# Kernel tuning notes

Measured on AMD Instinct MI355X. Metric: run time of the kernel, lower is better.

Reference implementation:

```python
import jax, jax.numpy as jnp
import numpy as np


def _rbf_forward(batches, centers, beta, W, b):
    # Pairwise Euclidean distances via GEMM expansion instead of materializing
    # the O(n*K*dim) difference tensor the torch code builds.
    x2 = jnp.sum(batches * batches, axis=1, keepdims=True)          # [n, 1]
    c2 = jnp.sum(centers * centers, axis=1)                          # [K]
    xc = jnp.einsum('nd,kd->nk', batches, centers)                   # [n, K]
    d2 = jnp.maximum(x2 + c2[None, :] - 2.0 * xc, 0.0)               # [n, K]
    dist = jnp.sqrt(d2)
    radial = jnp.exp(-beta * dist)                                   # beta: [1, K]
    return radial @ W.T + b                                          # [n, num_class]


def setup_inputs() -> dict:
    key = jax.random.key(0)
    k1, k2, k3, k4, k5 = jax.random.split(key, 5)
    n, K, dim, num_class = 16384, 2048, 512, 10
    batches = jax.random.normal(k1, (n, dim), dtype=jnp.float32)
    centers = jax.random.normal(k2, (K, dim), dtype=jnp.float32)
    beta = jnp.full((1, K), 0.1, dtype=jnp.float32)  # torch init: ones/10
    W = jax.random.normal(k4, (num_class, K), dtype=jnp.float32) / np.sqrt(K)
    b = jax.random.normal(k5, (num_class,), dtype=jnp.float32) * 0.01
    return {"batches": batches, "centers": centers, "beta": beta, "W": W, "b": b}


def reference(batches, centers, beta, W, b):
    return _rbf_forward(batches, centers, beta, W, b)
```

## Files before the change

kernel.cpp:

```cpp
#include <hip/hip_runtime.h>
#include <hip/hip_bf16.h>
#include <stdint.h>

#define M_N  16384
#define K_C  2048
#define DIM  512
#define NCLS 10
#define NBN  16
#define NBM  (M_N / 128)

typedef unsigned short u16;
typedef float  f32x4  __attribute__((ext_vector_type(4)));
typedef __bf16 bf16x8 __attribute__((ext_vector_type(8)));


__device__ __forceinline__ void async_ld16(const void* g, void* l) {
  __builtin_amdgcn_global_load_lds(
      (const __attribute__((address_space(1))) void*)g,
      (__attribute__((address_space(3))) void*)l,
      16, 0, 0);
}

__device__ __forceinline__ u16 f2bf_rne(float f) {
  uint32_t u = __float_as_uint(f);
  u += 0x7FFFu + ((u >> 16) & 1u);
  return (u16)(u >> 16);
}


#define NPREP ((M_N + K_C) / 2)

__global__ __launch_bounds__(256) void prep(
    const float4* __restrict__ batches, const float4* __restrict__ centers,
    const float* __restrict__ W,
    ushort4* __restrict__ Abf, ushort4* __restrict__ Bbf,
    float* __restrict__ x2, float* __restrict__ c2, u16* __restrict__ Wbf) {
  int b = blockIdx.x, t = threadIdx.x;
  if (b < NPREP) {
    int rp = b * 2 + (t >> 7);
    int col = t & 127;
    const float4* src; ushort4* dst; float* sq; int row;
    if (rp < M_N) { src = batches; dst = Abf; sq = x2; row = rp; }
    else          { src = centers; dst = Bbf; sq = c2; row = rp - M_N; }
    float4 v = src[(size_t)row * 128 + col];
    float ss = v.x * v.x + v.y * v.y + v.z * v.z + v.w * v.w;
    ushort4 o;
    o.x = f2bf_rne(v.x); o.y = f2bf_rne(v.y);
    o.z = f2bf_rne(v.z); o.w = f2bf_rne(v.w);
    dst[(size_t)row * 128 + col] = o;
    ss += __shfl_down(ss, 32);
    ss += __shfl_down(ss, 16);
    ss += __shfl_down(ss, 8);
    ss += __shfl_down(ss, 4);
    ss += __shfl_down(ss, 2);
    ss += __shfl_down(ss, 1);
    __shared__ float part[4];
    if ((t & 63) == 0) part[t >> 6] = ss;
    __syncthreads();
    if (t == 0) sq[row] = part[0] + part[1];
    if (t == 128) sq[row] = part[2] + part[3];
  } else {
    int wb = b - NPREP;
#pragma unroll
    for (int i = 0; i < 4; ++i) {
      int idx = wb * 1024 + i * 256 + t;
      int n = idx >> 11, k = idx & 2047;
      Wbf[idx] = (n < NCLS) ? f2bf_rne(W[n * K_C + k]) : (u16)0;
    }
  }
}


__global__ __launch_bounds__(256, 4) void rbf_main(
    const u16* __restrict__ A,
    const u16* __restrict__ B,
    const float* __restrict__ x2,
    const float* __restrict__ c2,
    const float* __restrict__ beta,
    const u16* __restrict__ Wbf,
    float* __restrict__ partial) {
  constexpr int BK = 64;
  __shared__ alignas(16) unsigned char smem[32768];
  u16* As = (u16*)smem;
  u16* Bs = (u16*)(smem + 16384);
  u16* Rt = (u16*)smem;

  const int tid  = threadIdx.x;
  const int lane = tid & 63;
  const int wid  = tid >> 6;
  const int bid = blockIdx.x;
  const int g = bid >> 3, r8 = bid & 7;
  const int bm = r8 * 16 + (g & 15);
  const int bn = g >> 4;
  const int row0 = bm * 128, col0 = bn * 128;
  const int wrC = (wid >> 1) * 64;
  const int wcB = (wid & 1) * 64;

  f32x4 acc[4][4] = {};

  const int srow = tid >> 3;
  const int scol = ((tid & 7) ^ (srow & 7)) * 8;
  const u16* aG = A + (size_t)(row0 + srow) * DIM + scol;
  const u16* bG = B + (size_t)(col0 + srow) * DIM + scol;
  u16* aL = As + tid * 8;
  u16* bL = Bs + tid * 8;

  const int frow = lane & 15;
  const int fq   = lane >> 4;
  const int fsw  = frow & 7;

  for (int k0 = 0; k0 < DIM; k0 += BK) {
    __syncthreads();
#pragma unroll
    for (int i = 0; i < 4; ++i) {
      async_ld16(aG + k0 + i * 32 * DIM, aL + i * 2048);
      async_ld16(bG + k0 + i * 32 * DIM, bL + i * 2048);
    }
    __syncthreads();

#pragma unroll
    for (int kh = 0; kh < 2; ++kh) {
      const int slot = ((kh << 2) | fq) ^ fsw;
      bf16x8 cf[4], bfr[4];
#pragma unroll
      for (int mi = 0; mi < 4; ++mi)
        cf[mi] = *(const bf16x8*)(Bs + (wrC + mi * 16 + frow) * BK + slot * 8);
#pragma unroll
      for (int ni = 0; ni < 4; ++ni)
        bfr[ni] = *(const bf16x8*)(As + (wcB + ni * 16 + frow) * BK + slot * 8);
#pragma unroll
      for (int mi = 0; mi < 4; ++mi)
#pragma unroll
        for (int ni = 0; ni < 4; ++ni)
          acc[mi][ni] = __builtin_amdgcn_mfma_f32_16x16x32_bf16(
              cf[mi], bfr[ni], acc[mi][ni], 0, 0, 0);
    }
  }

  const int cls = lane & 15, q = lane >> 4;
  float4 c2q[4], btq[4];
#pragma unroll
  for (int mi = 0; mi < 4; ++mi) {
    int base = col0 + wrC + mi * 16 + q * 4;
    c2q[mi] = *(const float4*)(c2 + base);
    btq[mi] = *(const float4*)(beta + base);
  }
  float x2v[4];
#pragma unroll
  for (int ni = 0; ni < 4; ++ni)
    x2v[ni] = x2[row0 + wcB + ni * 16 + cls];

  __syncthreads();

  union Pack { u16 h[4]; uint2 v; };
#pragma unroll
  for (int mi = 0; mi < 4; ++mi) {
#pragma unroll
    for (int ni = 0; ni < 4; ++ni) {
      Pack pk;
#pragma unroll
      for (int r = 0; r < 4; ++r) {
        float xc = acc[mi][ni][r];
        float d2 = fmaxf(x2v[ni] + c2q[mi][r] - 2.0f * xc, 0.0f);
        float radial = __expf(-btq[mi][r] * sqrtf(d2));
        pk.h[r] = f2bf_rne(radial);
      }
      int br  = wcB + ni * 16 + cls;
      int cc0 = wrC + mi * 16 + q * 4;
      *(uint2*)(Rt + br * 128 + (cc0 ^ ((br & 15) << 3))) = pk.v;
    }
  }
  __syncthreads();

  bf16x8 wfr[4];
#pragma unroll
  for (int t = 0; t < 4; ++t)
    wfr[t] = *(const bf16x8*)(Wbf + (size_t)cls * K_C + col0 + t * 32 + q * 8);

  f32x4 acc2[2] = {};
#pragma unroll
  for (int s2 = 0; s2 < 2; ++s2) {
    const int br = (wid * 2 + s2) * 16 + cls;
    const u16* rrow = Rt + br * 128;
    const int sw = cls << 3;
#pragma unroll
    for (int t = 0; t < 4; ++t) {
      bf16x8 ra = *(const bf16x8*)(rrow + ((t * 32 + q * 8) ^ sw));
      acc2[s2] = __builtin_amdgcn_mfma_f32_16x16x32_bf16(
          ra, wfr[t], acc2[s2], 0, 0, 0);
    }
  }

#pragma unroll
  for (int s2 = 0; s2 < 2; ++s2)
#pragma unroll
    for (int r = 0; r < 4; ++r) {
      int gr = row0 + (wid * 2 + s2) * 16 + q * 4 + r;
      partial[((size_t)bn * M_N + gr) * 16 + cls] = acc2[s2][r];
    }
}


__global__ __launch_bounds__(256) void reduce_out(
    const float* __restrict__ partial, const float* __restrict__ b,
    float* __restrict__ out) {
  int t = threadIdx.x;
  int row = blockIdx.x * 64 + (t >> 2);
  int quad = t & 3;
  float4 v = {0.f, 0.f, 0.f, 0.f};
#pragma unroll
  for (int bn = 0; bn < NBN; ++bn) {
    float4 p = *(const float4*)(partial + ((size_t)bn * M_N + row) * 16 + quad * 4);
    v.x += p.x; v.y += p.y; v.z += p.z; v.w += p.w;
  }
  if (quad == 0) {
    float4 bq = *(const float4*)b;
    float* o = out + (size_t)row * NCLS;
    *(float2*)o       = {v.x + bq.x, v.y + bq.y};
    *(float2*)(o + 2) = {v.z + bq.z, v.w + bq.w};
  } else if (quad == 1) {
    float4 bq = *(const float4*)(b + 4);
    float* o = out + (size_t)row * NCLS + 4;
    *(float2*)o       = {v.x + bq.x, v.y + bq.y};
    *(float2*)(o + 2) = {v.z + bq.z, v.w + bq.w};
  } else if (quad == 2) {
    *(float2*)(out + (size_t)row * NCLS + 8) = {v.x + b[8], v.y + b[9]};
  }
}


extern "C" void kernel_launch(void* const* d_in, const int* in_sizes, int n_in,
                              void* d_out, int out_size, void* d_ws, size_t ws_size,
                              hipStream_t stream) {
  const float* batches = (const float*)d_in[0];
  const float* centers = (const float*)d_in[1];
  const float* beta    = (const float*)d_in[2];
  const float* W       = (const float*)d_in[3];
  const float* bias    = (const float*)d_in[4];
  float* out = (float*)d_out;

  char* ws = (char*)d_ws;
  u16*  Abf = (u16*)ws;
  u16*  Bbf = (u16*)(ws + (size_t)M_N * DIM * 2);
  float* x2 = (float*)(ws + (size_t)(M_N + K_C) * DIM * 2);
  float* c2 = x2 + M_N;
  u16*  Wbf = (u16*)(c2 + K_C);
  float* partial = (float*)((char*)Wbf + 16 * K_C * 2);

  prep<<<dim3(NPREP + 32), dim3(256), 0, stream>>>(
      (const float4*)batches, (const float4*)centers, W,
      (ushort4*)Abf, (ushort4*)Bbf, x2, c2, Wbf);
  rbf_main<<<dim3(NBN * NBM), dim3(256), 0, stream>>>(
      Abf, Bbf, x2, c2, beta, Wbf, partial);
  reduce_out<<<dim3(M_N / 64), dim3(256), 0, stream>>>(partial, bias, out);
}
```

Baseline: 145.8 us.

## Feed radial values to second MFMA from registers via permuted W, skip LDS round-trip

```diff
diff --git a/kernel.cpp b/kernel.cpp
--- a/kernel.cpp
+++ b/kernel.cpp
@@ -34,7 +34,7 @@
     const float4* __restrict__ batches, const float4* __restrict__ centers,
     const float* __restrict__ W,
     ushort4* __restrict__ Abf, ushort4* __restrict__ Bbf,
-    float* __restrict__ x2, float* __restrict__ c2, u16* __restrict__ Wbf) {
+    float* __restrict__ x2, float* __restrict__ c2, u16* __restrict__ Wperm) {
   int b = blockIdx.x, t = threadIdx.x;
   if (b < NPREP) {
     int rp = b * 2 + (t >> 7);
@@ -63,9 +63,13 @@
     int wb = b - NPREP;
 #pragma unroll
     for (int i = 0; i < 4; ++i) {
-      int idx = wb * 1024 + i * 256 + t;
-      int n = idx >> 11, k = idx & 2047;
-      Wbf[idx] = (n < NCLS) ? f2bf_rne(W[n * K_C + k]) : (u16)0;
+      int p = wb * 1024 + i * 256 + t;
+      int cls = p >> 11, k = p & 2047;
+      int bn = k >> 7, rem = k & 127;
+      int hh = (rem >> 6) & 1, tt = (rem >> 5) & 1;
+      int qq = (rem >> 3) & 3, jj = rem & 7;
+      int c = bn * 128 + hh * 64 + (tt * 2 + (jj >> 2)) * 16 + qq * 4 + (jj & 3);
+      Wperm[p] = (cls < NCLS) ? f2bf_rne(W[cls * K_C + c]) : (u16)0;
     }
   }
 }
@@ -77,13 +81,13 @@
     const float* __restrict__ x2,
     const float* __restrict__ c2,
     const float* __restrict__ beta,
-    const u16* __restrict__ Wbf,
+    const u16* __restrict__ Wperm,
     float* __restrict__ partial) {
   constexpr int BK = 64;
   __shared__ alignas(16) unsigned char smem[32768];
   u16* As = (u16*)smem;
   u16* Bs = (u16*)(smem + 16384);
-  u16* Rt = (u16*)smem;
+  f32x4* sumbuf = (f32x4*)smem;
 
   const int tid  = threadIdx.x;
   const int lane = tid & 63;
@@ -150,54 +154,60 @@
   for (int ni = 0; ni < 4; ++ni)
     x2v[ni] = x2[row0 + wcB + ni * 16 + cls];
 
-  __syncthreads();
-
-  union Pack { u16 h[4]; uint2 v; };
-#pragma unroll
-  for (int mi = 0; mi < 4; ++mi) {
-#pragma unroll
-    for (int ni = 0; ni < 4; ++ni) {
-      Pack pk;
+#pragma unroll
+  for (int mi = 0; mi < 4; ++mi)
+#pragma unroll
+    for (int ni = 0; ni < 4; ++ni)
 #pragma unroll
       for (int r = 0; r < 4; ++r) {
         float xc = acc[mi][ni][r];
         float d2 = fmaxf(x2v[ni] + c2q[mi][r] - 2.0f * xc, 0.0f);
-        float radial = __expf(-btq[mi][r] * sqrtf(d2));
-        pk.h[r] = f2bf_rne(radial);
+        acc[mi][ni][r] = __expf(-btq[mi][r] * sqrtf(d2));
       }
-      int br  = wcB + ni * 16 + cls;
-      int cc0 = wrC + mi * 16 + q * 4;
-      *(uint2*)(Rt + br * 128 + (cc0 ^ ((br & 15) << 3))) = pk.v;
-    }
-  }
+
+  const int h = wid >> 1;
+  bf16x8 wfr[2];
+#pragma unroll
+  for (int t = 0; t < 2; ++t)
+    wfr[t] = *(const bf16x8*)(Wperm + (size_t)cls * K_C + col0 + h * 64 +
+                              t * 32 + q * 8);
+
+  f32x4 acc2[4] = {};
+#pragma unroll
+  for (int ni = 0; ni < 4; ++ni) {
+#pragma unroll
+    for (int t = 0; t < 2; ++t) {
+      union { u16 hh[8]; bf16x8 v; } pk;
+#pragma unroll
+      for (int r = 0; r < 4; ++r) {
+        pk.hh[r]     = f2bf_rne(acc[2 * t][ni][r]);
+        pk.hh[4 + r] = f2bf_rne(acc[2 * t + 1][ni][r]);
+      }
+      acc2[ni] = __builtin_amdgcn_mfma_f32_16x16x32_bf16(
+          pk.v, wfr[t], acc2[ni], 0, 0, 0);
+    }
+  }
+
   __syncthreads();
-
-  bf16x8 wfr[4];
-#pragma unroll
-  for (int t = 0; t < 4; ++t)
-    wfr[t] = *(const bf16x8*)(Wbf + (size_t)cls * K_C + col0 + t * 32 + q * 8);
-
-  f32x4 acc2[2] = {};
-#pragma unroll
-  for (int s2 = 0; s2 < 2; ++s2) {
-    const int br = (wid * 2 + s2) * 16 + cls;
-    const u16* rrow = Rt + br * 128;
-    const int sw = cls << 3;
-#pragma unroll
-    for (int t = 0; t < 4; ++t) {
-      bf16x8 ra = *(const bf16x8*)(rrow + ((t * 32 + q * 8) ^ sw));
-      acc2[s2] = __builtin_amdgcn_mfma_f32_16x16x32_bf16(
-          ra, wfr[t], acc2[s2], 0, 0, 0);
-    }
-  }
-
-#pragma unroll
-  for (int s2 = 0; s2 < 2; ++s2)
-#pragma unroll
-    for (int r = 0; r < 4; ++r) {
-      int gr = row0 + (wid * 2 + s2) * 16 + q * 4 + r;
-      partial[((size_t)bn * M_N + gr) * 16 + cls] = acc2[s2][r];
-    }
+  if (wid >= 2) {
+#pragma unroll
+    for (int ni = 0; ni < 4; ++ni)
+      sumbuf[((wid & 1) * 4 + ni) * 64 + lane] = acc2[ni];
+  }
+  __syncthreads();
+  if (wid < 2) {
+#pragma unroll
+    for (int ni = 0; ni < 4; ++ni) {
+      f32x4 o = sumbuf[(wid * 4 + ni) * 64 + lane];
+      acc2[ni] += o;
+#pragma unroll
+      for (int r = 0; r < 4; ++r) {
+        int gr = row0 + wid * 64 + ni * 16 + q * 4 + r;
+        __builtin_nontemporal_store(
+            acc2[ni][r], &partial[((size_t)bn * M_N + gr) * 16 + cls]);
+      }
+    }
+  }
 }
 
 
@@ -207,11 +217,12 @@
   int t = threadIdx.x;
   int row = blockIdx.x * 64 + (t >> 2);
   int quad = t & 3;
-  float4 v = {0.f, 0.f, 0.f, 0.f};
+  f32x4 v = {0.f, 0.f, 0.f, 0.f};
 #pragma unroll
   for (int bn = 0; bn < NBN; ++bn) {
-    float4 p = *(const float4*)(partial + ((size_t)bn * M_N + row) * 16 + quad * 4);
-    v.x += p.x; v.y += p.y; v.z += p.z; v.w += p.w;
+    f32x4 p = __builtin_nontemporal_load(
+        (const f32x4*)(partial + ((size_t)bn * M_N + row) * 16 + quad * 4));
+    v += p;
   }
   if (quad == 0) {
     float4 bq = *(const float4*)b;
@@ -244,13 +255,13 @@
   u16*  Bbf = (u16*)(ws + (size_t)M_N * DIM * 2);
   float* x2 = (float*)(ws + (size_t)(M_N + K_C) * DIM * 2);
   float* c2 = x2 + M_N;
-  u16*  Wbf = (u16*)(c2 + K_C);
-  float* partial = (float*)((char*)Wbf + 16 * K_C * 2);
+  u16*  Wpm = (u16*)(c2 + K_C);
+  float* partial = (float*)((char*)Wpm + 16 * K_C * 2);
 
   prep<<<dim3(NPREP + 32), dim3(256), 0, stream>>>(
       (const float4*)batches, (const float4*)centers, W,
-      (ushort4*)Abf, (ushort4*)Bbf, x2, c2, Wbf);
+      (ushort4*)Abf, (ushort4*)Bbf, x2, c2, Wpm);
   rbf_main<<<dim3(NBN * NBM), dim3(256), 0, stream>>>(
-      Abf, Bbf, x2, c2, beta, Wbf, partial);
+      Abf, Bbf, x2, c2, beta, Wpm, partial);
   reduce_out<<<dim3(M_N / 64), dim3(256), 0, stream>>>(partial, bias, out);
 }
```

Result: faster. 136.5 us (-6.4%).
